# Kernel optimization log

Hardware: AMD Instinct MI355X
Metric: run time of the kernel (lower is better)

Reference implementation:

```python
import jax, jax.numpy as jnp
import numpy as np

EMBED_DIM = 1024
NUM_HEADS = 16
HEAD_DIM = EMBED_DIM // NUM_HEADS
MLP_HIDDEN = 4096


def layer_norm(x, gamma, beta, eps=1e-5):
    mu = jnp.mean(x, axis=-1, keepdims=True)
    var = jnp.var(x, axis=-1, keepdims=True)
    return (x - mu) / jnp.sqrt(var + eps) * gamma + beta


def setup_inputs() -> dict:
    key = jax.random.key(0)
    ks = jax.random.split(key, 16)
    d, h = EMBED_DIM, MLP_HIDDEN
    s = 0.02
    inp = {
        "x": jax.random.normal(ks[0], (2, 2048, d), dtype=jnp.float32),
        "ln1_g": jnp.ones((d,), jnp.float32),
        "ln1_b": jnp.zeros((d,), jnp.float32),
        "ln2_g": jnp.ones((d,), jnp.float32),
        "ln2_b": jnp.zeros((d,), jnp.float32),
        "Wq": jax.random.normal(ks[1], (d, d), jnp.float32) * s,
        "bq": jnp.zeros((d,), jnp.float32),
        "Wk": jax.random.normal(ks[2], (d, d), jnp.float32) * s,
        "bk": jnp.zeros((d,), jnp.float32),
        "Wv": jax.random.normal(ks[3], (d, d), jnp.float32) * s,
        "bv": jnp.zeros((d,), jnp.float32),
        "Wo": jax.random.normal(ks[4], (d, d), jnp.float32) * s,
        "bo": jnp.zeros((d,), jnp.float32),
        "W1": jax.random.normal(ks[5], (d, h), jnp.float32) * s,
        "b1": jnp.zeros((h,), jnp.float32),
        "W2": jax.random.normal(ks[6], (h, d), jnp.float32) * s,
        "b2": jnp.zeros((d,), jnp.float32),
    }
    return inp


def reference(x, ln1_g, ln1_b, ln2_g, ln2_b, Wq, bq, Wk, bk, Wv, bv, Wo, bo, W1, b1, W2, b2):
    B, T, C = x.shape
    H, Dh = NUM_HEADS, HEAD_DIM
    # attention branch
    xn = layer_norm(x, ln1_g, ln1_b)
    q = (xn @ Wq + bq).reshape(B, T, H, Dh).transpose(0, 2, 1, 3)  # [B,H,T,Dh]
    k = (xn @ Wk + bk).reshape(B, T, H, Dh).transpose(0, 2, 1, 3)
    v = (xn @ Wv + bv).reshape(B, T, H, Dh).transpose(0, 2, 1, 3)
    scores = jnp.einsum('bhtd,bhsd->bhts', q, k) / jnp.sqrt(jnp.float32(Dh))
    attn = jax.nn.softmax(scores, axis=-1)
    out = jnp.einsum('bhts,bhsd->bhtd', attn, v)
    out = out.transpose(0, 2, 1, 3).reshape(B, T, C)
    x = x + out @ Wo + bo
    # MLP branch
    xn2 = layer_norm(x, ln2_g, ln2_b)
    x = x + jax.nn.relu(xn2 @ W1 + b1) @ W2 + b2
    return x
```

## Files before the change

### kernel.cpp

```cpp
#include <hip/hip_runtime.h>

typedef float f32x4 __attribute__((ext_vector_type(4)));
typedef __bf16 bf16x8 __attribute__((ext_vector_type(8)));

constexpr int TT   = 2048;
constexpr int CC   = 1024;
constexpr int HIDN = 4096;
constexpr int MM   = 4096;
constexpr int NQKV = 3072;

union U84 { uint32_t u[4]; bf16x8 v; };

__device__ inline uint32_t cvt_pk_bf16(float lo, float hi) {
  uint32_t r;
  asm("v_cvt_pk_bf16_f32 %0, %1, %2" : "=v"(r) : "v"(lo), "v"(hi));
  return r;
}
__device__ inline ushort f2bf(float f) { return (ushort)(cvt_pk_bf16(f, 0.f) & 0xffffu); }
__device__ inline float bfbits2f(uint32_t bits) {
  union { uint32_t u; float f; } c; c.u = bits; return c.f;
}
__device__ inline float exp2_fast(float x) {
  float r;
  asm("v_exp_f32 %0, %1" : "=v"(r) : "v"(x));
  return r;
}

#define AS1C(p) ((__attribute__((address_space(1))) void*)(p))
#define AS3(p)  ((__attribute__((address_space(3))) void*)(p))

__global__ __launch_bounds__(256) void prep_weights(const float* __restrict__ Wq,
                                                    const float* __restrict__ Wk,
                                                    const float* __restrict__ Wv,
                                                    const float* __restrict__ Wo,
                                                    const float* __restrict__ W1,
                                                    const float* __restrict__ W2,
                                                    const float* __restrict__ bq,
                                                    const float* __restrict__ bk,
                                                    const float* __restrict__ bv,
                                                    const float* __restrict__ x,
                                                    const float* __restrict__ g1,
                                                    const float* __restrict__ b1v,
                                                    ushort* __restrict__ WqkvT,
                                                    ushort* __restrict__ WoT,
                                                    ushort* __restrict__ W1T,
                                                    ushort* __restrict__ W2T,
                                                    float* __restrict__ Bqkv,
                                                    ushort* __restrict__ Xn) {
  const int id = blockIdx.x;
  const int t = threadIdx.x;
  if (id >= 12300) {
    const int row = id - 12300;
    float4 v = reinterpret_cast<const float4*>(x + (size_t)row * CC)[t];
    float s  = v.x + v.y + v.z + v.w;
    float ss = v.x * v.x + v.y * v.y + v.z * v.z + v.w * v.w;
#pragma unroll
    for (int off = 32; off; off >>= 1) {
      s  += __shfl_down(s, off);
      ss += __shfl_down(ss, off);
    }
    __shared__ float red[16];
    const int wid = t >> 6, lane = t & 63;
    if (lane == 0) { red[wid] = s; red[8 + wid] = ss; }
    __syncthreads();
    if (t == 0) {
      red[0] = red[0] + red[1] + red[2] + red[3];
      red[8] = red[8] + red[9] + red[10] + red[11];
    }
    __syncthreads();
    const float mu   = red[0] * (1.0f / CC);
    const float var  = red[8] * (1.0f / CC) - mu * mu;
    const float rstd = rsqrtf(var + 1e-5f);
    float4 gg = reinterpret_cast<const float4*>(g1)[t];
    float4 bb = reinterpret_cast<const float4*>(b1v)[t];
    uint2 st;
    st.x = cvt_pk_bf16((v.x - mu) * rstd * gg.x + bb.x, (v.y - mu) * rstd * gg.y + bb.y);
    st.y = cvt_pk_bf16((v.z - mu) * rstd * gg.z + bb.z, (v.w - mu) * rstd * gg.w + bb.w);
    *reinterpret_cast<uint2*>(Xn + (size_t)row * CC + t * 4) = st;
    return;
  }
  if (id >= 12288) {
    const int i = (id - 12288) * 256 + t;
    Bqkv[i] = (i < 1024) ? bq[i] : ((i < 2048) ? bk[i - 1024] : bv[i - 2048]);
    return;
  }
  const float* W; ushort* out; int Kd, Nd, bx, by, rowOff = 0;
  if (id < 4096) {
    const int which = id >> 10, sub = id & 1023;
    bx = sub & 31; by = sub >> 5; Kd = 1024; Nd = 1024;
    if (which == 0)      { W = Wq; out = WqkvT; rowOff = 0; }
    else if (which == 1) { W = Wk; out = WqkvT; rowOff = 1024; }
    else if (which == 2) { W = Wv; out = WqkvT; rowOff = 2048; }
    else                 { W = Wo; out = WoT; }
  } else if (id < 8192) {
    const int sub = id - 4096; bx = sub & 127; by = sub >> 7;
    W = W1; out = W1T; Kd = 1024; Nd = 4096;
  } else {
    const int sub = id - 8192; bx = sub & 31; by = sub >> 5;
    W = W2; out = W2T; Kd = 4096; Nd = 1024;
  }
  const int n0 = bx * 32, k0 = by * 32;
  __shared__ float Ts[32][33];
  {
    const int r = t >> 3, cb = (t & 7) * 4;
    float4 v = *reinterpret_cast<const float4*>(W + (size_t)(k0 + r) * Nd + n0 + cb);
    Ts[r][cb + 0] = v.x; Ts[r][cb + 1] = v.y; Ts[r][cb + 2] = v.z; Ts[r][cb + 3] = v.w;
  }
  __syncthreads();
  {
    const int nl = t >> 3, kb = (t & 7) * 4;
    uint2 st;
    st.x = cvt_pk_bf16(Ts[kb + 0][nl], Ts[kb + 1][nl]);
    st.y = cvt_pk_bf16(Ts[kb + 2][nl], Ts[kb + 3][nl]);
    *reinterpret_cast<uint2*>(out + (size_t)(rowOff + n0 + nl) * Kd + k0 + kb) = st;
  }
}

template <bool RELU, bool VOUT, bool PARTIAL>
__global__ __launch_bounds__(512, 2) void gemm_8w(const ushort* __restrict__ A,
                                                  const ushort* __restrict__ Bt,
                                                  const float* __restrict__ bias,
                                                  ushort* __restrict__ outp,
                                                  ushort* __restrict__ Vt,
                                                  ushort* __restrict__ P1,
                                                  ushort* __restrict__ P2,
                                                  ushort* __restrict__ P3,
                                                  int N, int K, int Kchunk) {
  __shared__ ushort lds[49152];
  const int t = threadIdx.x, lane = t & 63, w = t >> 6;
  const int g = lane >> 4, i16 = lane & 15;
  const int wr = w >> 2, wc = w & 3;
  const int nwg  = gridDim.x * gridDim.y;
  const int orig = blockIdx.y * gridDim.x + blockIdx.x;
  const int sw   = (orig & 7) * (nwg >> 3) + (orig >> 3);
  const int row0 = (sw / gridDim.x) * 256, col0 = (sw % gridDim.x) * 256;
  const int kstart = PARTIAL ? blockIdx.z * Kchunk : 0;
  const int NT = (PARTIAL ? Kchunk : K) >> 5;
  ushort* __restrict__ Out = outp;
  if (PARTIAL) Out = (blockIdx.z == 0) ? outp : (blockIdx.z == 1) ? P1
              : (blockIdx.z == 2) ? P2 : P3;

  const int c1 = t, c2 = t + 512;
  const int r1 = c1 >> 2, s1 = (c1 & 3) ^ ((r1 >> 1) & 3);
  const int r2 = c2 >> 2, s2 = (c2 & 3) ^ ((r2 >> 1) & 3);
  const ushort* aG1 = A + (size_t)(row0 + r1) * K + kstart + s1 * 8;
  const ushort* aG2 = A + (size_t)(row0 + r2) * K + kstart + s2 * 8;
  const ushort* bG1 = Bt + (size_t)(col0 + r1) * K + kstart + s1 * 8;
  const ushort* bG2 = Bt + (size_t)(col0 + r2) * K + kstart + s2 * 8;

  int aoff[8], boff[4];
#pragma unroll
  for (int mf = 0; mf < 8; ++mf) {
    const int R = wr * 128 + mf * 16 + i16;
    aoff[mf] = R * 64 + ((g ^ ((R >> 1) & 3)) << 4);
  }
#pragma unroll
  for (int nf = 0; nf < 4; ++nf) {
    const int Cn = wc * 64 + nf * 16 + i16;
    boff[nf] = Cn * 64 + ((g ^ ((Cn >> 1) & 3)) << 4);
  }

  f32x4 acc[8][4] = {};

  auto STAGE = [&](int bi, int kt) {
    char* aB = (char*)lds + bi * 32768;
    char* bB = aB + 16384;
    const int ko = kt * 32;
    __builtin_amdgcn_global_load_lds(AS1C(aG1 + ko), AS3(aB + w * 1024), 16, 0, 0);
    __builtin_amdgcn_global_load_lds(AS1C(aG2 + ko), AS3(aB + 8192 + w * 1024), 16, 0, 0);
    __builtin_amdgcn_global_load_lds(AS1C(bG1 + ko), AS3(bB + w * 1024), 16, 0, 0);
    __builtin_amdgcn_global_load_lds(AS1C(bG2 + ko), AS3(bB + 8192 + w * 1024), 16, 0, 0);
  };

  STAGE(0, 0);
  if (NT > 1) STAGE(1, 1);

  for (int kt = 0; kt < NT; ++kt) {
    const int cur = kt % 3;
    if (kt + 2 < NT) STAGE((kt + 2) % 3, kt + 2);
    if (kt + 2 < NT)      asm volatile("s_waitcnt vmcnt(8)" ::: "memory");
    else if (kt + 1 < NT) asm volatile("s_waitcnt vmcnt(4)" ::: "memory");
    else                  asm volatile("s_waitcnt vmcnt(0)" ::: "memory");
    asm volatile("s_barrier" ::: "memory");
    __builtin_amdgcn_sched_barrier(0);

    const char* aB = (const char*)lds + cur * 32768;
    const char* bB = aB + 16384;
    bf16x8 b4[4], a4[4];
#pragma unroll
    for (int nf = 0; nf < 4; ++nf) b4[nf] = *reinterpret_cast<const bf16x8*>(bB + boff[nf]);
#pragma unroll
    for (int mf = 0; mf < 4; ++mf) a4[mf] = *reinterpret_cast<const bf16x8*>(aB + aoff[mf]);
    __builtin_amdgcn_s_setprio(1);
#pragma unroll
    for (int mf = 0; mf < 4; ++mf)
#pragma unroll
      for (int nf = 0; nf < 4; ++nf)
        acc[mf][nf] = __builtin_amdgcn_mfma_f32_16x16x32_bf16(a4[mf], b4[nf], acc[mf][nf], 0, 0, 0);
    __builtin_amdgcn_s_setprio(0);
    asm volatile("s_barrier" ::: "memory");
    __builtin_amdgcn_sched_barrier(0);
#pragma unroll
    for (int mf = 0; mf < 4; ++mf) a4[mf] = *reinterpret_cast<const bf16x8*>(aB + aoff[mf + 4]);
    __builtin_amdgcn_s_setprio(1);
#pragma unroll
    for (int mf = 0; mf < 4; ++mf)
#pragma unroll
      for (int nf = 0; nf < 4; ++nf)
        acc[mf + 4][nf] = __builtin_amdgcn_mfma_f32_16x16x32_bf16(a4[mf], b4[nf], acc[mf + 4][nf], 0, 0, 0);
    __builtin_amdgcn_s_setprio(0);
    asm volatile("s_barrier" ::: "memory");
    __builtin_amdgcn_sched_barrier(0);
  }

  const int qcol0 = col0 + wc * 64;

  if (VOUT && qcol0 >= 2048) {
#pragma unroll
    for (int nf = 0; nf < 4; ++nf) {
      const int ncol = qcol0 + nf * 16 + i16;
      const float bb = bias[ncol];
      const int d = ncol - 2048;
      const int hh = d >> 6, dd = d & 63;
#pragma unroll
      for (int mf = 0; mf < 8; ++mf) {
        const int mrow = row0 + wr * 128 + mf * 16 + 4 * g;
        const int bb_ = mrow >> 11, tok = mrow & 2047;
        uint2 st;
        st.x = cvt_pk_bf16(acc[mf][nf][0] + bb, acc[mf][nf][1] + bb);
        st.y = cvt_pk_bf16(acc[mf][nf][2] + bb, acc[mf][nf][3] + bb);
        *reinterpret_cast<uint2*>(Vt + (size_t)((bb_ * 16 + hh) * 64 + dd) * TT + tok) = st;
      }
    }
    return;
  }

  float* Lf = (float*)((char*)lds + w * 4096);
  const int rr2 = lane >> 2, q = lane & 3;
#pragma unroll
  for (int mf = 0; mf < 8; ++mf) {
#pragma unroll
    for (int nf = 0; nf < 4; ++nf)
#pragma unroll
      for (int r = 0; r < 4; ++r) {
        const int row = 4 * g + r;
        Lf[row * 64 + ((16 * nf + i16) ^ ((row & 7) << 2))] = acc[mf][nf][r];
      }
    asm volatile("s_waitcnt lgkmcnt(0)" ::: "memory");
    uint32_t u[8];
#pragma unroll
    for (int j = 0; j < 4; ++j) {
      f32x4 v = *reinterpret_cast<const f32x4*>(Lf + rr2 * 64 + ((q * 16 + 4 * j) ^ ((rr2 & 7) << 2)));
      float e0 = v[0], e1 = v[1], e2 = v[2], e3 = v[3];
      if (!PARTIAL) {
        const float4 b4 = *reinterpret_cast<const float4*>(bias + qcol0 + q * 16 + 4 * j);
        e0 += b4.x; e1 += b4.y; e2 += b4.z; e3 += b4.w;
        if (RELU) {
          e0 = fmaxf(e0, 0.f); e1 = fmaxf(e1, 0.f);
          e2 = fmaxf(e2, 0.f); e3 = fmaxf(e3, 0.f);
        }
      }
      u[2 * j + 0] = cvt_pk_bf16(e0, e1);
      u[2 * j + 1] = cvt_pk_bf16(e2, e3);
    }
    const int mrow = row0 + wr * 128 + mf * 16 + rr2;
    ushort* orow = Out + (size_t)mrow * N + qcol0 + q * 16;
    uint4 s0; s0.x = u[0]; s0.y = u[1]; s0.z = u[2]; s0.w = u[3];
    uint4 s1; s1.x = u[4]; s1.y = u[5]; s1.z = u[6]; s1.w = u[7];
    *reinterpret_cast<uint4*>(orow) = s0;
    *reinterpret_cast<uint4*>(orow + 8) = s1;
    asm volatile("s_waitcnt lgkmcnt(0)" ::: "memory");
  }
}

__global__ __launch_bounds__(256) void gemm_splitk(const ushort* __restrict__ A,
                                                   const ushort* __restrict__ Bt,
                                                   ushort* __restrict__ P0,
                                                   ushort* __restrict__ P1,
                                                   ushort* __restrict__ P2,
                                                   ushort* __restrict__ P3,
                                                   int N, int K, int Kchunk) {
  __shared__ ushort Smem[8192];
  ushort* Asm = Smem;
  ushort* Bsm = Smem + 4096;
  const int t = threadIdx.x;
  const int lane = t & 63, w = t >> 6;
  const int g = lane >> 4, i16 = lane & 15;
  const int wrow = w >> 1, wcol = w & 1;
  const int nwg  = gridDim.x * gridDim.y;
  const int orig = blockIdx.y * gridDim.x + blockIdx.x;
  const int sw   = (orig & 7) * (nwg >> 3) + (orig >> 3);
  const int row0 = (sw / gridDim.x) * 128, col0 = (sw % gridDim.x) * 128;
  const int kstart = blockIdx.z * Kchunk;
  ushort* __restrict__ P = (blockIdx.z == 0) ? P0 : (blockIdx.z == 1) ? P1
                          : (blockIdx.z == 2) ? P2 : P3;

  f32x4 acc[4][4] = {};

  const int srow = t >> 2, sc = (t & 3) * 8;
  const ushort* aS1 = A + (size_t)(row0 + srow) * K + sc;
  const ushort* aS2 = A + (size_t)(row0 + 64 + srow) * K + sc;
  const ushort* bS1 = Bt + (size_t)(col0 + srow) * K + sc;
  const ushort* bS2 = Bt + (size_t)(col0 + 64 + srow) * K + sc;
  char* aL1 = (char*)Asm + w * 1024;
  char* aL2 = (char*)Asm + 4096 + w * 1024;
  char* bL1 = (char*)Bsm + w * 1024;
  char* bL2 = (char*)Bsm + 4096 + w * 1024;

  for (int k0 = kstart; k0 < kstart + Kchunk; k0 += 32) {
    __syncthreads();
    __builtin_amdgcn_global_load_lds(AS1C(aS1 + k0), AS3(aL1), 16, 0, 0);
    __builtin_amdgcn_global_load_lds(AS1C(aS2 + k0), AS3(aL2), 16, 0, 0);
    __builtin_amdgcn_global_load_lds(AS1C(bS1 + k0), AS3(bL1), 16, 0, 0);
    __builtin_amdgcn_global_load_lds(AS1C(bS2 + k0), AS3(bL2), 16, 0, 0);
    __syncthreads();

    bf16x8 a4[4], b4[4];
#pragma unroll
    for (int mf = 0; mf < 4; ++mf) {
      const int r = wrow * 64 + mf * 16 + i16;
      a4[mf] = *reinterpret_cast<const bf16x8*>((const char*)Asm + r * 64 + g * 16);
    }
#pragma unroll
    for (int nf = 0; nf < 4; ++nf) {
      const int c = wcol * 64 + nf * 16 + i16;
      b4[nf] = *reinterpret_cast<const bf16x8*>((const char*)Bsm + c * 64 + g * 16);
    }
#pragma unroll
    for (int mf = 0; mf < 4; ++mf)
#pragma unroll
      for (int nf = 0; nf < 4; ++nf)
        acc[mf][nf] = __builtin_amdgcn_mfma_f32_16x16x32_bf16(a4[mf], b4[nf], acc[mf][nf], 0, 0, 0);
  }

  __syncthreads();

  float* Lf = (float*)((char*)Smem + w * 4096);
  const int qcol0 = col0 + wcol * 64;
  const int rr = lane >> 2, q = lane & 3;
#pragma unroll
  for (int mf = 0; mf < 4; ++mf) {
#pragma unroll
    for (int nf = 0; nf < 4; ++nf)
#pragma unroll
      for (int r = 0; r < 4; ++r) {
        const int row = 4 * g + r;
        Lf[row * 64 + ((16 * nf + i16) ^ ((row & 7) << 2))] = acc[mf][nf][r];
      }
    asm volatile("s_waitcnt lgkmcnt(0)" ::: "memory");
    uint32_t u[8];
#pragma unroll
    for (int j = 0; j < 4; ++j) {
      f32x4 v = *reinterpret_cast<const f32x4*>(Lf + rr * 64 + ((q * 16 + 4 * j) ^ ((rr & 7) << 2)));
      u[2 * j + 0] = cvt_pk_bf16(v[0], v[1]);
      u[2 * j + 1] = cvt_pk_bf16(v[2], v[3]);
    }
    const int mrow = row0 + wrow * 64 + mf * 16 + rr;
    ushort* orow = P + (size_t)mrow * N + qcol0 + q * 16;
    uint4 s0; s0.x = u[0]; s0.y = u[1]; s0.z = u[2]; s0.w = u[3];
    uint4 s1; s1.x = u[4]; s1.y = u[5]; s1.z = u[6]; s1.w = u[7];
    *reinterpret_cast<uint4*>(orow) = s0;
    *reinterpret_cast<uint4*>(orow + 8) = s1;
    asm volatile("s_waitcnt lgkmcnt(0)" ::: "memory");
  }
}

__device__ inline float bfsum4(uint32_t a, uint32_t b, uint32_t c, uint32_t d, bool hi) {
  if (hi) return bfbits2f(a & 0xffff0000u) + bfbits2f(b & 0xffff0000u) +
                 bfbits2f(c & 0xffff0000u) + bfbits2f(d & 0xffff0000u);
  return bfbits2f(a << 16) + bfbits2f(b << 16) + bfbits2f(c << 16) + bfbits2f(d << 16);
}

__global__ __launch_bounds__(256) void reduce_wo_ln(const ushort* __restrict__ P0,
                                                    const ushort* __restrict__ P1,
                                                    const ushort* __restrict__ P2,
                                                    const ushort* __restrict__ P3,
                                                    const float* __restrict__ x,
                                                    const float* __restrict__ bo,
                                                    const float* __restrict__ g,
                                                    const float* __restrict__ b,
                                                    float* __restrict__ X1f,
                                                    ushort* __restrict__ Xn) {
  const int row = blockIdx.x, t = threadIdx.x;
  const size_t off = (size_t)row * CC + t * 4;
  float4 v  = *reinterpret_cast<const float4*>(x + off);
  const uint2 q0 = *reinterpret_cast<const uint2*>(P0 + off);
  const uint2 q1 = *reinterpret_cast<const uint2*>(P1 + off);
  const uint2 q2 = *reinterpret_cast<const uint2*>(P2 + off);
  const uint2 q3 = *reinterpret_cast<const uint2*>(P3 + off);
  float4 bb = reinterpret_cast<const float4*>(bo)[t];
  v.x += bfsum4(q0.x, q1.x, q2.x, q3.x, false) + bb.x;
  v.y += bfsum4(q0.x, q1.x, q2.x, q3.x, true)  + bb.y;
  v.z += bfsum4(q0.y, q1.y, q2.y, q3.y, false) + bb.z;
  v.w += bfsum4(q0.y, q1.y, q2.y, q3.y, true)  + bb.w;
  *reinterpret_cast<float4*>(X1f + off) = v;

  float s  = v.x + v.y + v.z + v.w;
  float ss = v.x * v.x + v.y * v.y + v.z * v.z + v.w * v.w;
#pragma unroll
  for (int o = 32; o; o >>= 1) {
    s  += __shfl_down(s, o);
    ss += __shfl_down(ss, o);
  }
  __shared__ float red[16];
  const int wid = t >> 6, lane = t & 63;
  if (lane == 0) { red[wid] = s; red[8 + wid] = ss; }
  __syncthreads();
  if (t == 0) {
    red[0] = red[0] + red[1] + red[2] + red[3];
    red[8] = red[8] + red[9] + red[10] + red[11];
  }
  __syncthreads();
  const float mu   = red[0] * (1.0f / CC);
  const float var  = red[8] * (1.0f / CC) - mu * mu;
  const float rstd = rsqrtf(var + 1e-5f);
  float4 gg = reinterpret_cast<const float4*>(g)[t];
  float4 lb = reinterpret_cast<const float4*>(b)[t];
  uint2 st;
  st.x = cvt_pk_bf16((v.x - mu) * rstd * gg.x + lb.x, (v.y - mu) * rstd * gg.y + lb.y);
  st.y = cvt_pk_bf16((v.z - mu) * rstd * gg.z + lb.z, (v.w - mu) * rstd * gg.w + lb.w);
  *reinterpret_cast<uint2*>(Xn + off) = st;
}

__global__ __launch_bounds__(256) void reduce_fc2(const ushort* __restrict__ P0,
                                                  const ushort* __restrict__ P1,
                                                  const ushort* __restrict__ P2,
                                                  const ushort* __restrict__ P3,
                                                  const float* __restrict__ X1,
                                                  const float* __restrict__ b2,
                                                  float* __restrict__ out) {
  const int row = blockIdx.x, t = threadIdx.x;
  const size_t off = (size_t)row * CC + t * 4;
  float4 v  = *reinterpret_cast<const float4*>(X1 + off);
  const uint2 q0 = *reinterpret_cast<const uint2*>(P0 + off);
  const uint2 q1 = *reinterpret_cast<const uint2*>(P1 + off);
  const uint2 q2 = *reinterpret_cast<const uint2*>(P2 + off);
  const uint2 q3 = *reinterpret_cast<const uint2*>(P3 + off);
  float4 bb = reinterpret_cast<const float4*>(b2)[t];
  v.x += bfsum4(q0.x, q1.x, q2.x, q3.x, false) + bb.x;
  v.y += bfsum4(q0.x, q1.x, q2.x, q3.x, true)  + bb.y;
  v.z += bfsum4(q0.y, q1.y, q2.y, q3.y, false) + bb.z;
  v.w += bfsum4(q0.y, q1.y, q2.y, q3.y, true)  + bb.w;
  *reinterpret_cast<float4*>(out + off) = v;
}

__global__ __launch_bounds__(512, 4) void attn_full(const ushort* __restrict__ qkv,
                                                    const ushort* __restrict__ Vt,
                                                    ushort* __restrict__ attnb) {
  __shared__ ushort Ks[2][4096];
  __shared__ ushort Vs[2][4096];
  __shared__ uint32_t Ps[8][16][36];
  const int t = threadIdx.x, lane = t & 63, w = t >> 6;
  const int g = lane >> 4, iq = lane & 15;
  const int flat = blockIdx.x;
  const int work = (flat & 7) * 64 + (flat >> 3);
  const int bh = work >> 4;
  const int qt = work & 15;
  const int b = bh >> 4, h = bh & 15;

  bf16x8 qfrag[2];
  {
    const ushort* qrow = qkv + (size_t)(b * TT + qt * 128 + w * 16 + iq) * NQKV + h * 64;
    const float qs = 0.125f * 1.44269504f;
#pragma unroll
    for (int kk = 0; kk < 2; ++kk) {
      uint4 raw = *reinterpret_cast<const uint4*>(qrow + kk * 32 + g * 8);
      uint32_t rr[4] = {raw.x, raw.y, raw.z, raw.w};
      U84 tmp;
#pragma unroll
      for (int c = 0; c < 4; ++c) {
        float lo = bfbits2f(rr[c] << 16) * qs;
        float hi = bfbits2f(rr[c] & 0xffff0000u) * qs;
        tmp.u[c] = cvt_pk_bf16(lo, hi);
      }
      qfrag[kk] = tmp.v;
    }
  }

  const int sr1 = t >> 3, sc1 = t & 7;
  const int csw = (sc1 ^ (sr1 & 7)) * 8;
  const ushort* kbase = qkv + 1024 + h * 64;
  const ushort* vbase = Vt + (size_t)(bh * 64) * TT;

  auto STAGE = [&](int bi, int kt) {
    const size_t tok = (size_t)(b * TT + kt * 64);
    __builtin_amdgcn_global_load_lds(AS1C(kbase + (tok + sr1) * NQKV + csw),
                                     AS3((char*)&Ks[bi][0] + w * 1024), 16, 0, 0);
    __builtin_amdgcn_global_load_lds(AS1C(vbase + (size_t)sr1 * TT + kt * 64 + csw),
                                     AS3((char*)&Vs[bi][0] + w * 1024), 16, 0, 0);
  };

  uint32_t (*pw)[36] = Ps[w];
  const int wsw = (iq & 8) << 1;
  const int xsb = wsw << 2;
  const char* prow = (const char*)&pw[iq][0];

  float lrun = 0.f;
  f32x4 ot[4] = {};

  constexpr int NKT = TT / 64;
  STAGE(0, 0);

  for (int kt = 0; kt < NKT; ++kt) {
    const int cur = kt & 1;
    if (kt + 1 < NKT) {
      STAGE(cur ^ 1, kt + 1);
      asm volatile("s_waitcnt vmcnt(2)" ::: "memory");
    } else {
      asm volatile("s_waitcnt vmcnt(0)" ::: "memory");
    }
    asm volatile("s_barrier" ::: "memory");
    __builtin_amdgcn_sched_barrier(0);
    const char* Kc = (const char*)&Ks[cur][0];
    const char* Vc = (const char*)&Vs[cur][0];

    f32x4 sfr[4] = {};
    __builtin_amdgcn_s_setprio(1);
#pragma unroll
    for (int kk = 0; kk < 2; ++kk)
#pragma unroll
      for (int jf = 0; jf < 4; ++jf) {
        const int row = iq + 16 * jf;
        const int off = row * 128 + ((kk * 64 + g * 16) ^ ((row & 7) << 4));
        bf16x8 a = *reinterpret_cast<const bf16x8*>(Kc + off);
        sfr[jf] = __builtin_amdgcn_mfma_f32_16x16x32_bf16(a, qfrag[kk], sfr[jf], 0, 0, 0);
      }
    __builtin_amdgcn_s_setprio(0);

#pragma unroll
    for (int f = 0; f < 4; ++f) {
      float p0 = exp2_fast(sfr[f][0]);
      float p1 = exp2_fast(sfr[f][1]);
      float p2 = exp2_fast(sfr[f][2]);
      float p3 = exp2_fast(sfr[f][3]);
      lrun += (p0 + p1) + (p2 + p3);
      uint2 st2;
      st2.x = cvt_pk_bf16(p0, p1);
      st2.y = cvt_pk_bf16(p2, p3);
      *reinterpret_cast<uint2*>(&pw[iq][(8 * f + 2 * g) ^ wsw]) = st2;
    }
    asm volatile("s_waitcnt lgkmcnt(0)" ::: "memory");

    __builtin_amdgcn_s_setprio(1);
#pragma unroll
    for (int kk = 0; kk < 2; ++kk) {
      bf16x8 pb = *reinterpret_cast<const bf16x8*>(prow + ((kk * 64 + g * 16) ^ xsb));
#pragma unroll
      for (int df = 0; df < 4; ++df) {
        const int row = iq + 16 * df;
        const int off = row * 128 + ((kk * 64 + g * 16) ^ ((row & 7) << 4));
        bf16x8 a = *reinterpret_cast<const bf16x8*>(Vc + off);
        ot[df] = __builtin_amdgcn_mfma_f32_16x16x32_bf16(a, pb, ot[df], 0, 0, 0);
      }
    }
    __builtin_amdgcn_s_setprio(0);

    asm volatile("s_barrier" ::: "memory");
    __builtin_amdgcn_sched_barrier(0);
  }

  lrun += __shfl_xor(lrun, 16, 64);
  lrun += __shfl_xor(lrun, 32, 64);
  const int grow = b * TT + qt * 128 + w * 16 + iq;
  const float inv = 1.f / lrun;
  ushort* orow = attnb + (size_t)grow * CC + h * 64;
#pragma unroll
  for (int df = 0; df < 4; ++df) {
    uint2 st;
    st.x = cvt_pk_bf16(ot[df][0] * inv, ot[df][1] * inv);
    st.y = cvt_pk_bf16(ot[df][2] * inv, ot[df][3] * inv);
    *reinterpret_cast<uint2*>(orow + df * 16 + g * 4) = st;
  }
}

extern "C" void kernel_launch(void* const* d_in, const int* in_sizes, int n_in,
                              void* d_out, int out_size, void* d_ws, size_t ws_size,
                              hipStream_t stream) {
  const float* x     = (const float*)d_in[0];
  const float* ln1_g = (const float*)d_in[1];
  const float* ln1_b = (const float*)d_in[2];
  const float* ln2_g = (const float*)d_in[3];
  const float* ln2_b = (const float*)d_in[4];
  const float* Wq = (const float*)d_in[5];
  const float* bq = (const float*)d_in[6];
  const float* Wk = (const float*)d_in[7];
  const float* bk = (const float*)d_in[8];
  const float* Wv = (const float*)d_in[9];
  const float* bv = (const float*)d_in[10];
  const float* Wo = (const float*)d_in[11];
  const float* bo = (const float*)d_in[12];
  const float* W1 = (const float*)d_in[13];
  const float* b1 = (const float*)d_in[14];
  const float* W2 = (const float*)d_in[15];
  const float* b2 = (const float*)d_in[16];
  float* out = (float*)d_out;
  char* ws = (char*)d_ws;

  ushort* WqkvT = (ushort*)(ws + 0);
  ushort* WoT   = (ushort*)(ws + 6291456);
  ushort* W1T   = (ushort*)(ws + 8388608);
  ushort* W2T   = (ushort*)(ws + 16777216);
  float*  Bqkv  = (float*) (ws + 25165824);
  ushort* Xn    = (ushort*)(ws + 25178112);
  ushort* Attn  = (ushort*)(ws + 33566720);
  float*  X1f   = (float*) (ws + 41955328);
  ushort* Qkv   = (ushort*)(ws + 58732544);
  ushort* Vtb   = (ushort*)(ws + 83898368);
  ushort* Hid   = (ushort*)(ws + 58732544);
  ushort* WoP0  = (ushort*)(ws + 58732544);
  ushort* WoP1  = (ushort*)(ws + 67121152);
  ushort* WoP2  = (ushort*)(ws + 75509760);
  ushort* WoP3  = (ushort*)(ws + 83898368);
  ushort* F2P0  = (ushort*)(ws + 0);
  ushort* F2P1  = (ushort*)(ws + 8388608);
  ushort* F2P2  = (ushort*)(ws + 25178112);
  ushort* F2P3  = (ushort*)(ws + 33566720);

  const dim3 blk(256);

  prep_weights<<<dim3(16396), blk, 0, stream>>>(Wq, Wk, Wv, Wo, W1, W2, bq, bk, bv,
                                                x, ln1_g, ln1_b,
                                                WqkvT, WoT, W1T, W2T, Bqkv, Xn);
  gemm_8w<false, true, false><<<dim3(12, 16), dim3(512), 0, stream>>>(
      Xn, WqkvT, Bqkv, Qkv, Vtb, nullptr, nullptr, nullptr, NQKV, 1024, 0);
  attn_full<<<dim3(512), dim3(512), 0, stream>>>(Qkv, Vtb, Attn);
  gemm_splitk<<<dim3(8, 32, 4), blk, 0, stream>>>(Attn, WoT, WoP0, WoP1, WoP2, WoP3, 1024, 1024, 256);
  reduce_wo_ln<<<dim3(MM), blk, 0, stream>>>(WoP0, WoP1, WoP2, WoP3, x, bo, ln2_g, ln2_b, X1f, Xn);
  gemm_8w<true, false, false><<<dim3(16, 16), dim3(512), 0, stream>>>(
      Xn, W1T, b1, Hid, nullptr, nullptr, nullptr, nullptr, HIDN, 1024, 0);
  gemm_8w<false, false, true><<<dim3(4, 16, 4), dim3(512), 0, stream>>>(
      Hid, W2T, nullptr, F2P0, nullptr, F2P1, F2P2, F2P3, 1024, 4096, 1024);
  reduce_fc2<<<dim3(MM), blk, 0, stream>>>(F2P0, F2P1, F2P2, F2P3, X1f, b2, out);
}
```

Baseline: 242.0 us.

## Double GEMM K-tile to 64 with double-buffered LDS and 8-way swizzle

Each GEMM main-loop iteration now stages a 64-wide K slice instead of 32, with a new 8-chunk XOR swizzle for 128-byte LDS rows. The triple-buffered pipeline is replaced by double buffering, which grows LDS from 96KB to 128KB. The intent is to halve barrier and loop overhead per unit of MFMA work and issue more loads per stage. In exchange, prefetch depth drops to one stage ahead, which may expose more memory latency.

```diff
diff --git a/kernel.cpp b/kernel.cpp
--- a/kernel.cpp
+++ b/kernel.cpp
@@ -126,7 +126,7 @@
                                                   ushort* __restrict__ P2,
                                                   ushort* __restrict__ P3,
                                                   int N, int K, int Kchunk) {
-  __shared__ ushort lds[49152];
+  __shared__ ushort lds[65536];
   const int t = threadIdx.x, lane = t & 63, w = t >> 6;
   const int g = lane >> 4, i16 = lane & 15;
   const int wr = w >> 2, wc = w & 3;
@@ -135,79 +135,101 @@
   const int sw   = (orig & 7) * (nwg >> 3) + (orig >> 3);
   const int row0 = (sw / gridDim.x) * 256, col0 = (sw % gridDim.x) * 256;
   const int kstart = PARTIAL ? blockIdx.z * Kchunk : 0;
-  const int NT = (PARTIAL ? Kchunk : K) >> 5;
+  const int NT = (PARTIAL ? Kchunk : K) >> 6;
   ushort* __restrict__ Out = outp;
   if (PARTIAL) Out = (blockIdx.z == 0) ? outp : (blockIdx.z == 1) ? P1
               : (blockIdx.z == 2) ? P2 : P3;
 
-  const int c1 = t, c2 = t + 512;
-  const int r1 = c1 >> 2, s1 = (c1 & 3) ^ ((r1 >> 1) & 3);
-  const int r2 = c2 >> 2, s2 = (c2 & 3) ^ ((r2 >> 1) & 3);
-  const ushort* aG1 = A + (size_t)(row0 + r1) * K + kstart + s1 * 8;
-  const ushort* aG2 = A + (size_t)(row0 + r2) * K + kstart + s2 * 8;
-  const ushort* bG1 = Bt + (size_t)(col0 + r1) * K + kstart + s1 * 8;
-  const ushort* bG2 = Bt + (size_t)(col0 + r2) * K + kstart + s2 * 8;
-
-  int aoff[8], boff[4];
+  const ushort* aG[4];
+  const ushort* bG[4];
+#pragma unroll
+  for (int i = 0; i < 4; ++i) {
+    const int c = t + 512 * i;
+    const int r = c >> 3, ssw = (c & 7) ^ (r & 7);
+    aG[i] = A  + (size_t)(row0 + r) * K + kstart + ssw * 8;
+    bG[i] = Bt + (size_t)(col0 + r) * K + kstart + ssw * 8;
+  }
+
+  int aoff[8][2], boff[4][2];
 #pragma unroll
   for (int mf = 0; mf < 8; ++mf) {
     const int R = wr * 128 + mf * 16 + i16;
-    aoff[mf] = R * 64 + ((g ^ ((R >> 1) & 3)) << 4);
+#pragma unroll
+    for (int kk = 0; kk < 2; ++kk)
+      aoff[mf][kk] = R * 128 + (((kk << 2) | g) ^ (R & 7)) * 16;
   }
 #pragma unroll
   for (int nf = 0; nf < 4; ++nf) {
     const int Cn = wc * 64 + nf * 16 + i16;
-    boff[nf] = Cn * 64 + ((g ^ ((Cn >> 1) & 3)) << 4);
+#pragma unroll
+    for (int kk = 0; kk < 2; ++kk)
+      boff[nf][kk] = Cn * 128 + (((kk << 2) | g) ^ (Cn & 7)) * 16;
   }
 
   f32x4 acc[8][4] = {};
 
   auto STAGE = [&](int bi, int kt) {
-    char* aB = (char*)lds + bi * 32768;
-    char* bB = aB + 16384;
-    const int ko = kt * 32;
-    __builtin_amdgcn_global_load_lds(AS1C(aG1 + ko), AS3(aB + w * 1024), 16, 0, 0);
-    __builtin_amdgcn_global_load_lds(AS1C(aG2 + ko), AS3(aB + 8192 + w * 1024), 16, 0, 0);
-    __builtin_amdgcn_global_load_lds(AS1C(bG1 + ko), AS3(bB + w * 1024), 16, 0, 0);
-    __builtin_amdgcn_global_load_lds(AS1C(bG2 + ko), AS3(bB + 8192 + w * 1024), 16, 0, 0);
+    char* aB = (char*)lds + bi * 65536;
+    char* bB = aB + 32768;
+    const int ko = kt * 64;
+#pragma unroll
+    for (int i = 0; i < 4; ++i)
+      __builtin_amdgcn_global_load_lds(AS1C(aG[i] + ko), AS3(aB + i * 8192 + w * 1024), 16, 0, 0);
+#pragma unroll
+    for (int i = 0; i < 4; ++i)
+      __builtin_amdgcn_global_load_lds(AS1C(bG[i] + ko), AS3(bB + i * 8192 + w * 1024), 16, 0, 0);
   };
 
   STAGE(0, 0);
-  if (NT > 1) STAGE(1, 1);
 
   for (int kt = 0; kt < NT; ++kt) {
-    const int cur = kt % 3;
-    if (kt + 2 < NT) STAGE((kt + 2) % 3, kt + 2);
-    if (kt + 2 < NT)      asm volatile("s_waitcnt vmcnt(8)" ::: "memory");
-    else if (kt + 1 < NT) asm volatile("s_waitcnt vmcnt(4)" ::: "memory");
-    else                  asm volatile("s_waitcnt vmcnt(0)" ::: "memory");
+    const int cur = kt & 1;
+    if (kt + 1 < NT) {
+      STAGE(cur ^ 1, kt + 1);
+      asm volatile("s_waitcnt vmcnt(8)" ::: "memory");
+    } else {
+      asm volatile("s_waitcnt vmcnt(0)" ::: "memory");
+    }
     asm volatile("s_barrier" ::: "memory");
     __builtin_amdgcn_sched_barrier(0);
 
-    const char* aB = (const char*)lds + cur * 32768;
-    const char* bB = aB + 16384;
-    bf16x8 b4[4], a4[4];
-#pragma unroll
-    for (int nf = 0; nf < 4; ++nf) b4[nf] = *reinterpret_cast<const bf16x8*>(bB + boff[nf]);
-#pragma unroll
-    for (int mf = 0; mf < 4; ++mf) a4[mf] = *reinterpret_cast<const bf16x8*>(aB + aoff[mf]);
+    const char* aB = (const char*)lds + cur * 65536;
+    const char* bB = aB + 32768;
+    bf16x8 b4[4][2], a4[4][2];
+#pragma unroll
+    for (int nf = 0; nf < 4; ++nf)
+#pragma unroll
+      for (int kk = 0; kk < 2; ++kk)
+        b4[nf][kk] = *reinterpret_cast<const bf16x8*>(bB + boff[nf][kk]);
+#pragma unroll
+    for (int mf = 0; mf < 4; ++mf)
+#pragma unroll
+      for (int kk = 0; kk < 2; ++kk)
+        a4[mf][kk] = *reinterpret_cast<const bf16x8*>(aB + aoff[mf][kk]);
     __builtin_amdgcn_s_setprio(1);
 #pragma unroll
     for (int mf = 0; mf < 4; ++mf)
 #pragma unroll
       for (int nf = 0; nf < 4; ++nf)
-        acc[mf][nf] = __builtin_amdgcn_mfma_f32_16x16x32_bf16(a4[mf], b4[nf], acc[mf][nf], 0, 0, 0);
+#pragma unroll
+        for (int kk = 0; kk < 2; ++kk)
+          acc[mf][nf] = __builtin_amdgcn_mfma_f32_16x16x32_bf16(a4[mf][kk], b4[nf][kk], acc[mf][nf], 0, 0, 0);
     __builtin_amdgcn_s_setprio(0);
     asm volatile("s_barrier" ::: "memory");
     __builtin_amdgcn_sched_barrier(0);
 #pragma unroll
-    for (int mf = 0; mf < 4; ++mf) a4[mf] = *reinterpret_cast<const bf16x8*>(aB + aoff[mf + 4]);
+    for (int mf = 0; mf < 4; ++mf)
+#pragma unroll
+      for (int kk = 0; kk < 2; ++kk)
+        a4[mf][kk] = *reinterpret_cast<const bf16x8*>(aB + aoff[mf + 4][kk]);
     __builtin_amdgcn_s_setprio(1);
 #pragma unroll
     for (int mf = 0; mf < 4; ++mf)
 #pragma unroll
       for (int nf = 0; nf < 4; ++nf)
-        acc[mf + 4][nf] = __builtin_amdgcn_mfma_f32_16x16x32_bf16(a4[mf], b4[nf], acc[mf + 4][nf], 0, 0, 0);
+#pragma unroll
+        for (int kk = 0; kk < 2; ++kk)
+          acc[mf + 4][nf] = __builtin_amdgcn_mfma_f32_16x16x32_bf16(a4[mf][kk], b4[nf][kk], acc[mf + 4][nf], 0, 0, 0);
     __builtin_amdgcn_s_setprio(0);
     asm volatile("s_barrier" ::: "memory");
     __builtin_amdgcn_sched_barrier(0);
@@ -253,8 +275,8 @@
       f32x4 v = *reinterpret_cast<const f32x4*>(Lf + rr2 * 64 + ((q * 16 + 4 * j) ^ ((rr2 & 7) << 2)));
       float e0 = v[0], e1 = v[1], e2 = v[2], e3 = v[3];
       if (!PARTIAL) {
-        const float4 b4 = *reinterpret_cast<const float4*>(bias + qcol0 + q * 16 + 4 * j);
-        e0 += b4.x; e1 += b4.y; e2 += b4.z; e3 += b4.w;
+        const float4 b4v = *reinterpret_cast<const float4*>(bias + qcol0 + q * 16 + 4 * j);
+        e0 += b4v.x; e1 += b4v.y; e2 += b4v.z; e3 += b4v.w;
         if (RELU) {
           e0 = fmaxf(e0, 0.f); e1 = fmaxf(e1, 0.f);
           e2 = fmaxf(e2, 0.f); e3 = fmaxf(e3, 0.f);
```

Measured after the change: 234.4 us. -3.2%, faster.
